# Optimization experiments

Measured on AMD Instinct MI355X. Metric: run time of the kernel, lower is better.

Reference implementation:

```python
import jax, jax.numpy as jnp
import numpy as np

V, N = 3, 32768
C2, C3 = 256, 32          # feat_ch_2D, feat_ch_3D
H = W = 128               # 2D feature map size
D = 32                    # 3D volume feature size
CIN = C2 + C3             # 288, MLP in_channels


def setup_inputs() -> dict:
    key = jax.random.key(0)
    ks = jax.random.split(key, 16)
    sc = 0.02
    inp = {
        'pts': jax.random.uniform(ks[0], (1, N, 3), minval=-0.5, maxval=0.5),
        'pts_proj': jax.random.uniform(ks[1], (1, N, 2), minval=-1.0, maxval=1.0),
        'img_feat0': jax.random.normal(ks[2], (V, C2, H, W)),
        'img_feat1': jax.random.normal(ks[3], (V, C2, H, W)),
        'vol_feat0': jax.random.normal(ks[4], (V, C3, D, D, D)),
        'vol_feat1': jax.random.normal(ks[5], (V, C3, D, D, D)),
        'W0': jax.random.normal(ks[6], (1024, CIN)) * sc,  'b0': jnp.zeros((1024,)),
        'W1': jax.random.normal(ks[7], (512, CIN + 1024)) * sc, 'b1': jnp.zeros((512,)),
        'W2': jax.random.normal(ks[8], (256, CIN + 512)) * sc,  'b2': jnp.zeros((256,)),
        'W3': jax.random.normal(ks[9], (128, CIN + 256)) * sc,  'b3': jnp.zeros((128,)),
        'W4': jax.random.normal(ks[10], (1, 128)) * sc,         'b4': jnp.zeros((1,)),
        'mean_num': 3,
    }
    return inp


def _gs2d(feat, gx, gy):
    # feat: [C,H,W]; gx,gy: [N] normalized coords in [-1,1]
    C, Hh, Ww = feat.shape
    ix = jnp.clip(((gx + 1.0) * Ww - 1.0) * 0.5, 0.0, Ww - 1.0)  # align_corners=False, border pad
    iy = jnp.clip(((gy + 1.0) * Hh - 1.0) * 0.5, 0.0, Hh - 1.0)
    x0f, y0f = jnp.floor(ix), jnp.floor(iy)
    wx, wy = ix - x0f, iy - y0f
    x0 = x0f.astype(jnp.int32); x1 = jnp.minimum(x0 + 1, Ww - 1)
    y0 = y0f.astype(jnp.int32); y1 = jnp.minimum(y0 + 1, Hh - 1)
    v00 = feat[:, y0, x0]; v01 = feat[:, y0, x1]
    v10 = feat[:, y1, x0]; v11 = feat[:, y1, x1]
    return (v00 * (1 - wy) * (1 - wx) + v01 * (1 - wy) * wx
            + v10 * wy * (1 - wx) + v11 * wy * wx)  # [C,N]


def _gs3d(feat, gx, gy, gz):
    # feat: [C,D,H,W]; grid x->W, y->H, z->D (torch grid_sample convention)
    C, Dd, Hh, Ww = feat.shape
    ix = jnp.clip(((gx + 1.0) * Ww - 1.0) * 0.5, 0.0, Ww - 1.0)
    iy = jnp.clip(((gy + 1.0) * Hh - 1.0) * 0.5, 0.0, Hh - 1.0)
    iz = jnp.clip(((gz + 1.0) * Dd - 1.0) * 0.5, 0.0, Dd - 1.0)
    x0f, y0f, z0f = jnp.floor(ix), jnp.floor(iy), jnp.floor(iz)
    wx, wy, wz = ix - x0f, iy - y0f, iz - z0f
    x0 = x0f.astype(jnp.int32); x1 = jnp.minimum(x0 + 1, Ww - 1)
    y0 = y0f.astype(jnp.int32); y1 = jnp.minimum(y0 + 1, Hh - 1)
    z0 = z0f.astype(jnp.int32); z1 = jnp.minimum(z0 + 1, Dd - 1)
    def g(zi, yi, xi):
        return feat[:, zi, yi, xi]  # [C,N]
    out = (g(z0, y0, x0) * (1 - wz) * (1 - wy) * (1 - wx)
           + g(z0, y0, x1) * (1 - wz) * (1 - wy) * wx
           + g(z0, y1, x0) * (1 - wz) * wy * (1 - wx)
           + g(z0, y1, x1) * (1 - wz) * wy * wx
           + g(z1, y0, x0) * wz * (1 - wy) * (1 - wx)
           + g(z1, y0, x1) * wz * (1 - wy) * wx
           + g(z1, y1, x0) * wz * wy * (1 - wx)
           + g(z1, y1, x1) * wz * wy * wx)
    return out  # [C,N]


def _lrelu(x):
    return jnp.where(x >= 0, x, 0.2 * x)


def _conv1x1(Wm, bm, x):
    # x: [V,C,N] -> [V,O,N]
    return jnp.einsum('oc,vcn->von', Wm, x) + bm[None, :, None]


def _mlp0(x, W0, b0, W1, b1, W2, b2, W3, b3):
    out = _lrelu(_conv1x1(W0, b0, x))
    out = _lrelu(_conv1x1(W1, b1, jnp.concatenate([x, out], axis=1)))
    out = _lrelu(_conv1x1(W2, b2, jnp.concatenate([x, out], axis=1)))
    out = _lrelu(_conv1x1(W3, b3, jnp.concatenate([x, out], axis=1)))
    return out  # [V,128,N]


def _forward(pts, pts_proj, img_feats, vol_feats,
             W0, b0, W1, b1, W2, b2, W3, b3, W4, b4, mean_num):
    v = img_feats[0].shape[0]
    gx2 = jnp.broadcast_to(pts_proj[:, :, 0], (v, pts_proj.shape[1]))
    gy2 = jnp.broadcast_to(pts_proj[:, :, 1], (v, pts_proj.shape[1]))
    p = pts * 2.0  # pts *= 2.0 before 3D sampling
    gx3 = jnp.broadcast_to(p[:, :, 0], (v, p.shape[1]))
    gy3 = jnp.broadcast_to(p[:, :, 1], (v, p.shape[1]))
    gz3 = jnp.broadcast_to(p[:, :, 2], (v, p.shape[1]))
    outs = []
    for img_feat, vol_feat in zip(img_feats, vol_feats):
        f2 = jax.vmap(_gs2d)(img_feat, gx2, gy2)            # [V,C2,N]
        f3 = jax.vmap(_gs3d)(vol_feat, gx3, gy3, gz3)       # [V,C3,N]
        pt_feat = jnp.concatenate([f2, f3], axis=1)         # [V,288,N]
        pt_out0 = _mlp0(pt_feat, W0, b0, W1, b1, W2, b2, W3, b3)
        pt_out0_mean = jnp.mean(pt_out0[:mean_num], axis=0, keepdims=True)  # [1,128,N]
        sdf = jax.nn.sigmoid(_conv1x1(W4, b4, pt_out0_mean))                # [1,1,N]
        outs.append(jnp.transpose(sdf, (0, 2, 1)))                          # [1,N,1]
    return tuple(outs)


def reference(pts, pts_proj, img_feat0, img_feat1, vol_feat0, vol_feat1,
              W0, b0, W1, b1, W2, b2, W3, b3, W4, b4, mean_num):
    return _forward(pts, pts_proj, [img_feat0, img_feat1], [vol_feat0, vol_feat1],
                    W0, b0, W1, b1, W2, b2, W3, b3, W4, b4, mean_num)
```

## Files before the change

### kernel.cpp

```cpp
#include <hip/hip_runtime.h>
#include <hip/hip_bf16.h>

#define NV 3
#define NPTS 32768
#define C2C 256
#define C3C 32
#define CINC 288
#define CINP 320
#define HH 128
#define WWW 128
#define DDD 32

typedef short bh8 __attribute__((ext_vector_type(8)));
typedef float fx4 __attribute__((ext_vector_type(4)));
typedef unsigned short us4 __attribute__((ext_vector_type(4)));

__device__ __forceinline__ float b2f(unsigned short u) {
    unsigned int x = ((unsigned int)u) << 16;
    return __uint_as_float(x);
}
__device__ __forceinline__ unsigned short f2b(float f) {
    unsigned int x = __float_as_uint(f);
    unsigned int r = (x + 0x7FFFu + ((x >> 16) & 1u)) >> 16;
    return (unsigned short)r;
}

__device__ __forceinline__ void gl2lds16(const unsigned short* g, unsigned short* l) {
    __builtin_amdgcn_global_load_lds(
        (const __attribute__((address_space(1))) unsigned int*)g,
        (__attribute__((address_space(3))) unsigned int*)l, 16, 0, 0);
}

template <int MB>
__device__ __forceinline__ void pair_decode(int b, int& mIdx, int& nIdx) {
    constexpr int L = (MB == 1) ? 0 : (MB == 2) ? 1 : 2;
    nIdx = ((b >> (3 + L)) << 3) | (b & 7);
    mIdx = (b >> 3) & (MB - 1);
}

__global__ __launch_bounds__(256) void k_prep(
    const float* __restrict__ s0, const float* __restrict__ s1,
    const float* __restrict__ s2, const float* __restrict__ s3,
    unsigned short* __restrict__ d0, unsigned short* __restrict__ d1,
    unsigned short* __restrict__ d2, unsigned short* __restrict__ d3,
    const float* __restrict__ img0, const float* __restrict__ img1,
    unsigned short* __restrict__ imgT, size_t imgStride,
    const float* __restrict__ vol0, const float* __restrict__ vol1,
    unsigned short* __restrict__ volT, size_t volStride) {
    __shared__ float smem[32 * 257];
    int b = blockIdx.x;
    if (b < 5088) {
        int base, M, Kp;
        const float* src;
        unsigned short* dst;
        if (b < 1280)      { base = 0;    M = 1024; Kp = 320;  src = s0; dst = d0; }
        else if (b < 3968) { base = 1280; M = 512;  Kp = 1344; src = s1; dst = d1; }
        else if (b < 4800) { base = 3968; M = 256;  Kp = 832;  src = s2; dst = d2; }
        else               { base = 4800; M = 128;  Kp = 576;  src = s3; dst = d3; }
        int idx = (b - base) * 256 + threadIdx.x;
        if (idx >= M * Kp) return;
        int m = idx / Kp, k = idx - m * Kp;
        int Ksrc = Kp - 32;
        float v;
        if (k < CINC) v = src[(size_t)m * Ksrc + k];
        else if (k < CINP) v = 0.0f;
        else v = src[(size_t)m * Ksrc + (k - 32)];
        dst[idx] = f2b(v);
    } else if (b < 11232) {
        int id = b - 5088;
        int bx = id % 384, by = (id / 384) & 1, bz = id / 768;
        int lvl = bz >> 2, cb = bz & 3;
        const float* in = lvl ? img1 : img0;
        int v = bx >> 7, y = bx & 127;
        int x0 = by << 6, c0 = cb << 6;
        float (*t)[65] = (float(*)[65])smem;
        int tx = threadIdx.x & 63, tg = threadIdx.x >> 6;
        const float* src = in + (((size_t)(v * C2C + c0) * HH + y) * WWW + x0);
#pragma unroll
        for (int i = 0; i < 16; i++) {
            int cl = tg * 16 + i;
            t[cl][tx] = src[(size_t)cl * (HH * WWW) + tx];
        }
        __syncthreads();
        unsigned short* dst = imgT + lvl * imgStride + ((size_t)(v * HH + y) * WWW + x0) * C2C + c0;
#pragma unroll
        for (int i = 0; i < 16; i++) {
            int xl = tg * 16 + i;
            dst[(size_t)xl * C2C + tx] = f2b(t[tx][xl]);
        }
    } else {
        int id = b - 11232;
        int v = id % 3, sy = (id / 3) & 127, lvl = id / 384;
        const float* in = lvl ? vol1 : vol0;
        int s0i = sy << 8;
        float (*t)[257] = (float(*)[257])smem;
        int tid = threadIdx.x;
        const float* src = in + (size_t)v * C3C * 32768 + s0i;
#pragma unroll
        for (int c = 0; c < 32; c++) t[c][tid] = src[(size_t)c * 32768 + tid];
        __syncthreads();
        unsigned short* dst = volT + lvl * volStride + ((size_t)v * 32768 + s0i) * C3C;
        int c = tid & 31, sb = tid >> 5;
#pragma unroll
        for (int j = 0; j < 32; j++) {
            int sl = j * 8 + sb;
            dst[(size_t)sl * C3C + c] = f2b(t[c][sl]);
        }
    }
}

__device__ __forceinline__ void sample_body(const float* __restrict__ pts, const float* __restrict__ proj,
                         const unsigned short* __restrict__ imgT, const unsigned short* __restrict__ volT,
                         unsigned short* __restrict__ ptT, int n0, int Nk) {
    int w = threadIdx.x >> 6, l = threadIdx.x & 63;
    int i = blockIdx.x * 4 + w;
    int v = blockIdx.y;
    int n = n0 + i;
    unsigned short* dstRow = ptT + (size_t)(v * Nk + i) * CINP;

    {
        float gx = proj[n * 2 + 0], gy = proj[n * 2 + 1];
        float ix = fminf(fmaxf(((gx + 1.0f) * (float)WWW - 1.0f) * 0.5f, 0.0f), (float)(WWW - 1));
        float iy = fminf(fmaxf(((gy + 1.0f) * (float)HH - 1.0f) * 0.5f, 0.0f), (float)(HH - 1));
        float x0f = floorf(ix), y0f = floorf(iy);
        float wx = ix - x0f, wy = iy - y0f;
        int x0 = (int)x0f, y0 = (int)y0f;
        int x1 = min(x0 + 1, WWW - 1), y1 = min(y0 + 1, HH - 1);
        const unsigned short* base = imgT + (size_t)v * HH * WWW * C2C;
        us4 a = *((const us4*)(base + ((size_t)(y0 * WWW + x0)) * C2C) + l);
        us4 b = *((const us4*)(base + ((size_t)(y0 * WWW + x1)) * C2C) + l);
        us4 c = *((const us4*)(base + ((size_t)(y1 * WWW + x0)) * C2C) + l);
        us4 d = *((const us4*)(base + ((size_t)(y1 * WWW + x1)) * C2C) + l);
        float w00 = (1.0f - wy) * (1.0f - wx), w01 = (1.0f - wy) * wx;
        float w10 = wy * (1.0f - wx), w11 = wy * wx;
        us4 rv;
#pragma unroll
        for (int r = 0; r < 4; r++) {
            float f = b2f(a[r]) * w00 + b2f(b[r]) * w01 + b2f(c[r]) * w10 + b2f(d[r]) * w11;
            rv[r] = f2b(f);
        }
        *(us4*)(dstRow + l * 4) = rv;
    }
    {
        float gx = pts[n * 3 + 0] * 2.0f, gy = pts[n * 3 + 1] * 2.0f, gz = pts[n * 3 + 2] * 2.0f;
        float ix = fminf(fmaxf(((gx + 1.0f) * (float)DDD - 1.0f) * 0.5f, 0.0f), (float)(DDD - 1));
        float iy = fminf(fmaxf(((gy + 1.0f) * (float)DDD - 1.0f) * 0.5f, 0.0f), (float)(DDD - 1));
        float iz = fminf(fmaxf(((gz + 1.0f) * (float)DDD - 1.0f) * 0.5f, 0.0f), (float)(DDD - 1));
        float x0f = floorf(ix), y0f = floorf(iy), z0f = floorf(iz);
        float wx = ix - x0f, wy = iy - y0f, wz = iz - z0f;
        int x0 = (int)x0f, y0 = (int)y0f, z0 = (int)z0f;
        int x1 = min(x0 + 1, DDD - 1), y1 = min(y0 + 1, DDD - 1), z1 = min(z0 + 1, DDD - 1);
        int c = l & 31, zs = l >> 5;
        int zi = zs ? z1 : z0;
        float wzs = zs ? wz : (1.0f - wz);
        const unsigned short* base = volT + (size_t)v * 32768 * C3C;
        float f00 = b2f(base[((size_t)((zi * 32 + y0) * 32 + x0)) * C3C + c]);
        float f01 = b2f(base[((size_t)((zi * 32 + y0) * 32 + x1)) * C3C + c]);
        float f10 = b2f(base[((size_t)((zi * 32 + y1) * 32 + x0)) * C3C + c]);
        float f11 = b2f(base[((size_t)((zi * 32 + y1) * 32 + x1)) * C3C + c]);
        float r = (f00 * (1.0f - wy) * (1.0f - wx) + f01 * (1.0f - wy) * wx +
                   f10 * wy * (1.0f - wx) + f11 * wy * wx) * wzs;
        float other = __shfl_xor(r, 32);
        r += other;
        if (zs == 0) dstRow[C2C + c] = f2b(r);
    }
    if (l < 8) *(us4*)(dstRow + CINC + l * 4) = (us4){0, 0, 0, 0};
}

__global__ __launch_bounds__(256) void k_sampleL0(const float* p, const float* pr, const unsigned short* im,
                                                  const unsigned short* vo, unsigned short* pt, int n0, int Nk) {
    sample_body(p, pr, im, vo, pt, n0, Nk);
}
__global__ __launch_bounds__(256) void k_sampleL1(const float* p, const float* pr, const unsigned short* im,
                                                  const unsigned short* vo, unsigned short* pt, int n0, int Nk) {
    sample_body(p, pr, im, vo, pt, n0, Nk);
}

template <int K2, int M, int MB>
__device__ __forceinline__ void gemm128_body(const unsigned short* __restrict__ A,
                                             const unsigned short* __restrict__ B1,
                                             const unsigned short* __restrict__ B2,
                                             const float* __restrict__ bias,
                                             unsigned short* __restrict__ C) {
    constexpr int K1 = CINP;
    constexpr int K = K1 + K2;
    constexpr int nt1 = K1 / 32;
    constexpr int nt = K / 32;
    __shared__ unsigned short Ash[3][128 * 32];
    __shared__ unsigned short Bsh[3][128 * 32];
    int tid = threadIdx.x;
    int w = tid >> 6, l = tid & 63;
    int la = l & 15, lg = l >> 4;
    int wm = w & 1, wn = w >> 1;
    int mIdx, nIdx;
    pair_decode<MB>(blockIdx.x, mIdx, nIdx);
    int mBlk = mIdx * 128;
    int nBlk = nIdx * 128;
    int sRow = l >> 2, sCol = (l & 3) * 8;
    int r0 = w * 32 + sRow, r1 = r0 + 16;

    const unsigned short* Ag = A + (size_t)mBlk * K;
    const unsigned short* B1g = B1 + (size_t)nBlk * K1;
    const unsigned short* B2g = (K2 > 0) ? (B2 + (size_t)nBlk * K2) : (const unsigned short*)0;

    fx4 acc[4][4];
#pragma unroll
    for (int mi = 0; mi < 4; mi++)
#pragma unroll
        for (int ni = 0; ni < 4; ni++) acc[mi][ni] = (fx4){0.f, 0.f, 0.f, 0.f};

    auto stage = [&](int t, int b) {
        const unsigned short* as = Ag + t * 32 + sCol;
        gl2lds16(as + (size_t)r0 * K, &Ash[b][r0 * 32 + sCol]);
        gl2lds16(as + (size_t)r1 * K, &Ash[b][r1 * 32 + sCol]);
        const unsigned short* bs;
        size_t ldb;
        if (t < nt1) { bs = B1g + t * 32 + sCol; ldb = (size_t)K1; }
        else         { bs = B2g + (t - nt1) * 32 + sCol; ldb = (size_t)K2; }
        gl2lds16(bs + (size_t)r0 * ldb, &Bsh[b][r0 * 32 + sCol]);
        gl2lds16(bs + (size_t)r1 * ldb, &Bsh[b][r1 * 32 + sCol]);
    };

    stage(0, 0);
    if (nt > 1) stage(1, 1);
    asm volatile("s_waitcnt vmcnt(4)" ::: "memory");
    __builtin_amdgcn_s_barrier();
    int cur = 0, nxt2 = 2;
    for (int t = 0; t < nt; t++) {
        if (t + 2 < nt) stage(t + 2, nxt2);
        bh8 af[4], bfv[4];
#pragma unroll
        for (int mi = 0; mi < 4; mi++) af[mi] = *(const bh8*)&Ash[cur][(wm * 64 + mi * 16 + la) * 32 + lg * 8];
#pragma unroll
        for (int ni = 0; ni < 4; ni++) bfv[ni] = *(const bh8*)&Bsh[cur][(wn * 64 + ni * 16 + la) * 32 + lg * 8];
#pragma unroll
        for (int mi = 0; mi < 4; mi++)
#pragma unroll
            for (int ni = 0; ni < 4; ni++)
                acc[mi][ni] = __builtin_amdgcn_mfma_f32_16x16x32_bf16(af[mi], bfv[ni], acc[mi][ni], 0, 0, 0);
        asm volatile("s_waitcnt lgkmcnt(0)" ::: "memory");
        if (t + 2 < nt)      asm volatile("s_waitcnt vmcnt(4)" ::: "memory");
        else if (t + 1 < nt) asm volatile("s_waitcnt vmcnt(0)" ::: "memory");
        __builtin_amdgcn_s_barrier();
        cur = (cur == 2) ? 0 : cur + 1;
        nxt2 = (nxt2 == 2) ? 0 : nxt2 + 1;
    }

#pragma unroll
    for (int mi = 0; mi < 4; mi++) {
        int m0 = mBlk + wm * 64 + mi * 16 + lg * 4;
        fx4 bb = *(const fx4*)(bias + m0);
#pragma unroll
        for (int ni = 0; ni < 4; ni++) {
            int n = nBlk + wn * 64 + ni * 16 + la;
            us4 rv;
#pragma unroll
            for (int r = 0; r < 4; r++) {
                float x = acc[mi][ni][r] + bb[r];
                x = (x >= 0.0f) ? x : 0.2f * x;
                rv[r] = f2b(x);
            }
            *(us4*)(C + (size_t)n * M + m0) = rv;
        }
    }
}

__global__ __launch_bounds__(256) void k_g2L0(const unsigned short* A, const unsigned short* B1, const unsigned short* B2,
                                              const float* b, unsigned short* C) { gemm128_body<512, 256, 2>(A, B1, B2, b, C); }
__global__ __launch_bounds__(256) void k_g2L1(const unsigned short* A, const unsigned short* B1, const unsigned short* B2,
                                              const float* b, unsigned short* C) { gemm128_body<512, 256, 2>(A, B1, B2, b, C); }
__global__ __launch_bounds__(256) void k_g3L0(const unsigned short* A, const unsigned short* B1, const unsigned short* B2,
                                              const float* b, unsigned short* C) { gemm128_body<256, 128, 1>(A, B1, B2, b, C); }
__global__ __launch_bounds__(256) void k_g3L1(const unsigned short* A, const unsigned short* B1, const unsigned short* B2,
                                              const float* b, unsigned short* C) { gemm128_body<256, 128, 1>(A, B1, B2, b, C); }

template <int KP, int K2, int M, int MB>
__device__ __forceinline__ void g1t_body(const unsigned short* __restrict__ A,
                                         const unsigned short* __restrict__ B1,
                                         const unsigned short* __restrict__ B2,
                                         const float* __restrict__ bias,
                                         unsigned short* __restrict__ C) {
    constexpr int nt = KP >> 6;
    __shared__ unsigned short As[2][256 * 64];
    __shared__ unsigned short Bs[2][256 * 64];
    int tid = threadIdx.x;
    int w = tid >> 6, l = tid & 63;
    int la = l & 15, lg = l >> 4;
    int wm = w >> 2, wn = w & 3;
    int mIdx, nIdx;
    pair_decode<MB>(blockIdx.x, mIdx, nIdx);
    int mBlk = mIdx * 256;
    int nBlk = nIdx * 256;

    const unsigned short* Ag = A + (size_t)mBlk * KP;

    fx4 acc[8][4];
#pragma unroll
    for (int mi = 0; mi < 8; mi++)
#pragma unroll
        for (int ni = 0; ni < 4; ni++) acc[mi][ni] = (fx4){0.f, 0.f, 0.f, 0.f};

    auto stageB = [&](int t, int nxt) {
        const unsigned short* bsrc;
        size_t ldb;
        int kc;
        if (t < 5) { bsrc = B1; ldb = CINP; kc = t * 64; }
        else       { bsrc = B2; ldb = (size_t)K2; kc = (t - 5) * 64; }
        bsrc += (size_t)nBlk * ldb + kc;
#pragma unroll
        for (int h = 0; h < 2; h++)
#pragma unroll
            for (int j = 0; j < 2; j++) {
                int idx = j * 512 + tid;
                int r = (h << 7) + (idx >> 3);
                int c = (idx & 7) ^ (r & 7);
                gl2lds16(bsrc + (size_t)r * ldb + c * 8, &Bs[nxt][(h << 13) + idx * 8]);
            }
    };
    auto stageA1 = [&](int t, int nxt) {
        const unsigned short* asrc = Ag + t * 64;
#pragma unroll
        for (int h = 0; h < 2; h++) {
            int idx = tid;
            int r = (h << 7) + (idx >> 3);
            int c = (idx & 7) ^ (r & 7);
            gl2lds16(asrc + (size_t)r * KP + c * 8, &As[nxt][(h << 13) + idx * 8]);
        }
    };
    auto stageA2 = [&](int t, int nxt) {
        const unsigned short* asrc = Ag + t * 64;
#pragma unroll
        for (int h = 0; h < 2; h++) {
            int idx = 512 + tid;
            int r = (h << 7) + (idx >> 3);
            int c = (idx & 7) ^ (r & 7);
            gl2lds16(asrc + (size_t)r * KP + c * 8, &As[nxt][(h << 13) + idx * 8]);
        }
    };

    stageB(0, 0);
    stageA1(0, 0);
    stageA2(0, 0);
    asm volatile("s_waitcnt vmcnt(0)" ::: "memory");
    __builtin_amdgcn_s_barrier();

    for (int t = 0; t < nt; t++) {
        int cur = t & 1;
        const unsigned short* Ab = &As[cur][0];
        const unsigned short* Bb = &Bs[cur][0];
        bh8 afr[4][2];
#pragma unroll
        for (int p = 0; p < 4; p++) {
            int qm = p >> 1, qn = p & 1;
            if (qn == 0) {
#pragma unroll
                for (int m2 = 0; m2 < 4; m2++)
#pragma unroll
                    for (int s = 0; s < 2; s++) {
                        int row = wm * 128 + (qm * 4 + m2) * 16 + la;
                        int c = (s * 4 + lg) ^ (row & 7);
                        afr[m2][s] = *(const bh8*)&Ab[row * 64 + c * 8];
                    }
            }
            bh8 bfr[2][2];
#pragma unroll
            for (int n2 = 0; n2 < 2; n2++)
#pragma unroll
                for (int s = 0; s < 2; s++) {
                    int row = wn * 64 + (qn * 2 + n2) * 16 + la;
                    int c = (s * 4 + lg) ^ (row & 7);
                    bfr[n2][s] = *(const bh8*)&Bb[row * 64 + c * 8];
                }
            if (p == 0 && t + 1 < nt) stageB(t + 1, cur ^ 1);
            if (p == 1 && t + 1 < nt) stageA1(t + 1, cur ^ 1);
            if (p == 2 && t + 1 < nt) stageA2(t + 1, cur ^ 1);
            __builtin_amdgcn_s_barrier();
            __builtin_amdgcn_s_setprio(1);
#pragma unroll
            for (int m2 = 0; m2 < 4; m2++)
#pragma unroll
                for (int n2 = 0; n2 < 2; n2++)
#pragma unroll
                    for (int s = 0; s < 2; s++)
                        acc[qm * 4 + m2][qn * 2 + n2] = __builtin_amdgcn_mfma_f32_16x16x32_bf16(
                            afr[m2][s], bfr[n2][s], acc[qm * 4 + m2][qn * 2 + n2], 0, 0, 0);
            __builtin_amdgcn_s_setprio(0);
            if (p == 1) {
                if (t + 1 < nt) asm volatile("s_waitcnt vmcnt(6)" ::: "memory");
                else            asm volatile("s_waitcnt vmcnt(0)" ::: "memory");
            }
            if (p == 3) {
                asm volatile("s_waitcnt lgkmcnt(0)" ::: "memory");
                if (t + 1 < nt) asm volatile("s_waitcnt vmcnt(2)" ::: "memory");
            }
            __builtin_amdgcn_s_barrier();
        }
    }

#pragma unroll
    for (int mi = 0; mi < 8; mi++) {
        int m0 = mBlk + wm * 128 + mi * 16 + lg * 4;
        fx4 bb = *(const fx4*)(bias + m0);
#pragma unroll
        for (int ni = 0; ni < 4; ni++) {
            int n = nBlk + wn * 64 + ni * 16 + la;
            us4 rv;
#pragma unroll
            for (int r = 0; r < 4; r++) {
                float x = acc[mi][ni][r] + bb[r];
                x = (x >= 0.0f) ? x : 0.2f * x;
                rv[r] = f2b(x);
            }
            *(us4*)(C + (size_t)n * M + m0) = rv;
        }
    }
}

__global__ __launch_bounds__(512) void k_g0L0(const unsigned short* A, const unsigned short* B1,
                                              const float* b, unsigned short* C) { g1t_body<320, 0, 1024, 4>(A, B1, nullptr, b, C); }
__global__ __launch_bounds__(512) void k_g0L1(const unsigned short* A, const unsigned short* B1,
                                              const float* b, unsigned short* C) { g1t_body<320, 0, 1024, 4>(A, B1, nullptr, b, C); }
__global__ __launch_bounds__(512) void k_g1L0(const unsigned short* A, const unsigned short* B1, const unsigned short* B2,
                                              const float* b, unsigned short* C) { g1t_body<1344, 1024, 512, 2>(A, B1, B2, b, C); }
__global__ __launch_bounds__(512) void k_g1L1(const unsigned short* A, const unsigned short* B1, const unsigned short* B2,
                                              const float* b, unsigned short* C) { g1t_body<1344, 1024, 512, 2>(A, B1, B2, b, C); }

__device__ __forceinline__ void head_body(const unsigned short* __restrict__ o3, const float* __restrict__ W4,
                       const float* __restrict__ b4, const int* __restrict__ mn_p,
                       float* __restrict__ out, int n0, int Nk, int level) {
    int wv = threadIdx.x >> 6, l = threadIdx.x & 63;
    int sub = l >> 4, cl = l & 15;
    int i = blockIdx.x * 16 + wv * 4 + sub;
    if (i >= Nk) return;
    int mn = *mn_p;
    if (mn > NV) mn = NV;
    if (mn < 1) mn = 1;
    fx4 w0 = *(const fx4*)(W4 + cl * 8);
    fx4 w1 = *(const fx4*)(W4 + cl * 8 + 4);
    float s = 0.0f;
    for (int v = 0; v < mn; v++) {
        bh8 x = *(const bh8*)(o3 + (size_t)(v * Nk + i) * 128 + cl * 8);
#pragma unroll
        for (int r = 0; r < 4; r++) s += w0[r] * b2f((unsigned short)x[r]);
#pragma unroll
        for (int r = 0; r < 4; r++) s += w1[r] * b2f((unsigned short)x[4 + r]);
    }
#pragma unroll
    for (int m = 1; m < 16; m <<= 1) s += __shfl_xor(s, m);
    if (cl == 0) {
        s = s / (float)mn + b4[0];
        out[(size_t)level * NPTS + n0 + i] = 1.0f / (1.0f + expf(-s));
    }
}

__global__ __launch_bounds__(256) void k_headL0(const unsigned short* o3, const float* W4, const float* b4,
                                                const int* mn, float* out, int n0, int Nk) {
    head_body(o3, W4, b4, mn, out, n0, Nk, 0);
}
__global__ __launch_bounds__(256) void k_headL1(const unsigned short* o3, const float* W4, const float* b4,
                                                const int* mn, float* out, int n0, int Nk) {
    head_body(o3, W4, b4, mn, out, n0, Nk, 1);
}

extern "C" void kernel_launch(void* const* d_in, const int* in_sizes, int n_in,
                              void* d_out, int out_size, void* d_ws, size_t ws_size,
                              hipStream_t stream) {
    const float* pts = (const float*)d_in[0];
    const float* proj = (const float*)d_in[1];
    const float* img[2] = {(const float*)d_in[2], (const float*)d_in[3]};
    const float* vol[2] = {(const float*)d_in[4], (const float*)d_in[5]};
    const float* Wf[4] = {(const float*)d_in[6], (const float*)d_in[8], (const float*)d_in[10], (const float*)d_in[12]};
    const float* bf[4] = {(const float*)d_in[7], (const float*)d_in[9], (const float*)d_in[11], (const float*)d_in[13]};
    const float* W4 = (const float*)d_in[14];
    const float* b4 = (const float*)d_in[15];
    const int* mn = (const int*)d_in[16];
    float* out = (float*)d_out;

    const int Kp[4] = {320, 1344, 832, 576};
    const int Msz[4] = {1024, 512, 256, 128};

    char* ws = (char*)d_ws;
    size_t off = 0;
    auto alloc = [&](size_t bytes) -> char* {
        char* p = ws + off;
        off = (off + bytes + 255) & ~(size_t)255;
        return p;
    };

    const size_t imgStride = (size_t)NV * HH * WWW * C2C;
    const size_t volStride = (size_t)NV * 32768 * C3C;

    unsigned short* Wb[4];
    for (int i = 0; i < 4; i++) Wb[i] = (unsigned short*)alloc((size_t)Msz[i] * Kp[i] * 2);
    unsigned short* imgT = (unsigned short*)alloc(2 * imgStride * 2);
    unsigned short* volT = (unsigned short*)alloc(2 * volStride * 2);
    size_t fixed = off;

    const size_t perPt = (size_t)NV * 2 * (CINP + 1024 + 512);
    int Nk = NPTS;
    if (fixed + (size_t)Nk * perPt + 4096 > ws_size) {
        size_t avail = (ws_size > fixed + 4096) ? (ws_size - fixed - 4096) : 0;
        long nk = (long)(avail / perPt);
        nk = (nk / 512) * 512;
        if (nk < 512) nk = 512;
        if (nk > NPTS) nk = NPTS;
        Nk = (int)nk;
    }
    unsigned short* ptT = (unsigned short*)alloc((size_t)NV * Nk * CINP * 2);
    unsigned short* o0 = (unsigned short*)alloc((size_t)NV * Nk * 1024 * 2);
    unsigned short* o1 = (unsigned short*)alloc((size_t)NV * Nk * 512 * 2);
    unsigned short* o2 = o0;
    unsigned short* o3 = o0 + (size_t)NV * Nk * 256;

    k_prep<<<12000, 256, 0, stream>>>(Wf[0], Wf[1], Wf[2], Wf[3], Wb[0], Wb[1], Wb[2], Wb[3],
                                      img[0], img[1], imgT, imgStride, vol[0], vol[1], volT, volStride);

    for (int n0 = 0; n0 < NPTS; n0 += Nk) {
        int nk = NPTS - n0 < Nk ? NPTS - n0 : Nk;
        int NC = NV * nk;
        int nP256 = NC / 256;
        int nP128 = NC / 128;
        k_sampleL0<<<dim3(nk / 4, NV), 256, 0, stream>>>(pts, proj, imgT, volT, ptT, n0, nk);
        k_g0L0<<<4 * nP256, 512, 0, stream>>>(Wb[0], ptT, bf[0], o0);
        k_g1L0<<<2 * nP256, 512, 0, stream>>>(Wb[1], ptT, o0, bf[1], o1);
        k_g2L0<<<2 * nP128, 256, 0, stream>>>(Wb[2], ptT, o1, bf[2], o2);
        k_g3L0<<<1 * nP128, 256, 0, stream>>>(Wb[3], ptT, o2, bf[3], o3);
        k_headL0<<<(nk + 15) / 16, 256, 0, stream>>>(o3, W4, b4, mn, out, n0, nk);
        k_sampleL1<<<dim3(nk / 4, NV), 256, 0, stream>>>(pts, proj, imgT + imgStride, volT + volStride, ptT, n0, nk);
        k_g0L1<<<4 * nP256, 512, 0, stream>>>(Wb[0], ptT, bf[0], o0);
        k_g1L1<<<2 * nP256, 512, 0, stream>>>(Wb[1], ptT, o0, bf[1], o1);
        k_g2L1<<<2 * nP128, 256, 0, stream>>>(Wb[2], ptT, o1, bf[2], o2);
        k_g3L1<<<1 * nP128, 256, 0, stream>>>(Wb[3], ptT, o2, bf[3], o3);
        k_headL1<<<(nk + 15) / 16, 256, 0, stream>>>(o3, W4, b4, mn, out, n0, nk);
    }
}
```

Before: 1.071 ms.

## Fuse final head dot product into layer-3 GEMM epilogue and retile layer 2

New measurement: 1.027 ms. 4.1% less time.

```diff
diff --git a/kernel.cpp b/kernel.cpp
--- a/kernel.cpp
+++ b/kernel.cpp
@@ -176,32 +176,31 @@
     sample_body(p, pr, im, vo, pt, n0, Nk);
 }
 
-template <int K2, int M, int MB>
-__device__ __forceinline__ void gemm128_body(const unsigned short* __restrict__ A,
-                                             const unsigned short* __restrict__ B1,
-                                             const unsigned short* __restrict__ B2,
-                                             const float* __restrict__ bias,
-                                             unsigned short* __restrict__ C) {
+template <int K2>
+__device__ __forceinline__ void g3dot_body(const unsigned short* __restrict__ A,
+                                           const unsigned short* __restrict__ B1,
+                                           const unsigned short* __restrict__ B2,
+                                           const float* __restrict__ bias,
+                                           const float* __restrict__ W4v,
+                                           float* __restrict__ dout) {
     constexpr int K1 = CINP;
     constexpr int K = K1 + K2;
     constexpr int nt1 = K1 / 32;
     constexpr int nt = K / 32;
     __shared__ unsigned short Ash[3][128 * 32];
     __shared__ unsigned short Bsh[3][128 * 32];
+    __shared__ float ds[128];
     int tid = threadIdx.x;
     int w = tid >> 6, l = tid & 63;
     int la = l & 15, lg = l >> 4;
     int wm = w & 1, wn = w >> 1;
-    int mIdx, nIdx;
-    pair_decode<MB>(blockIdx.x, mIdx, nIdx);
-    int mBlk = mIdx * 128;
-    int nBlk = nIdx * 128;
+    int nBlk = blockIdx.x * 128;
     int sRow = l >> 2, sCol = (l & 3) * 8;
     int r0 = w * 32 + sRow, r1 = r0 + 16;
 
-    const unsigned short* Ag = A + (size_t)mBlk * K;
+    const unsigned short* Ag = A;
     const unsigned short* B1g = B1 + (size_t)nBlk * K1;
-    const unsigned short* B2g = (K2 > 0) ? (B2 + (size_t)nBlk * K2) : (const unsigned short*)0;
+    const unsigned short* B2g = B2 + (size_t)nBlk * K2;
 
     fx4 acc[4][4];
 #pragma unroll
@@ -246,33 +245,34 @@
         nxt2 = (nxt2 == 2) ? 0 : nxt2 + 1;
     }
 
-#pragma unroll
-    for (int mi = 0; mi < 4; mi++) {
-        int m0 = mBlk + wm * 64 + mi * 16 + lg * 4;
-        fx4 bb = *(const fx4*)(bias + m0);
-#pragma unroll
-        for (int ni = 0; ni < 4; ni++) {
-            int n = nBlk + wn * 64 + ni * 16 + la;
-            us4 rv;
+    if (tid < 128) ds[tid] = 0.0f;
+    __syncthreads();
+#pragma unroll
+    for (int ni = 0; ni < 4; ni++) {
+        float part = 0.0f;
+#pragma unroll
+        for (int mi = 0; mi < 4; mi++) {
+            int m0 = wm * 64 + mi * 16 + lg * 4;
+            fx4 bb = *(const fx4*)(bias + m0);
 #pragma unroll
             for (int r = 0; r < 4; r++) {
                 float x = acc[mi][ni][r] + bb[r];
                 x = (x >= 0.0f) ? x : 0.2f * x;
-                rv[r] = f2b(x);
+                part += W4v[m0 + r] * x;
             }
-            *(us4*)(C + (size_t)n * M + m0) = rv;
-        }
-    }
-}
-
-__global__ __launch_bounds__(256) void k_g2L0(const unsigned short* A, const unsigned short* B1, const unsigned short* B2,
-                                              const float* b, unsigned short* C) { gemm128_body<512, 256, 2>(A, B1, B2, b, C); }
-__global__ __launch_bounds__(256) void k_g2L1(const unsigned short* A, const unsigned short* B1, const unsigned short* B2,
-                                              const float* b, unsigned short* C) { gemm128_body<512, 256, 2>(A, B1, B2, b, C); }
+        }
+        part += __shfl_xor(part, 16);
+        part += __shfl_xor(part, 32);
+        if (lg == 0) atomicAdd(&ds[wn * 64 + ni * 16 + la], part);
+    }
+    __syncthreads();
+    if (tid < 128) dout[nBlk + tid] = ds[tid];
+}
+
 __global__ __launch_bounds__(256) void k_g3L0(const unsigned short* A, const unsigned short* B1, const unsigned short* B2,
-                                              const float* b, unsigned short* C) { gemm128_body<256, 128, 1>(A, B1, B2, b, C); }
+                                              const float* b, const float* W4, float* dout) { g3dot_body<256>(A, B1, B2, b, W4, dout); }
 __global__ __launch_bounds__(256) void k_g3L1(const unsigned short* A, const unsigned short* B1, const unsigned short* B2,
-                                              const float* b, unsigned short* C) { gemm128_body<256, 128, 1>(A, B1, B2, b, C); }
+                                              const float* b, const float* W4, float* dout) { g3dot_body<256>(A, B1, B2, b, W4, dout); }
 
 template <int KP, int K2, int M, int MB>
 __device__ __forceinline__ void g1t_body(const unsigned short* __restrict__ A,
@@ -424,42 +424,23 @@
                                               const float* b, unsigned short* C) { g1t_body<1344, 1024, 512, 2>(A, B1, B2, b, C); }
 __global__ __launch_bounds__(512) void k_g1L1(const unsigned short* A, const unsigned short* B1, const unsigned short* B2,
                                               const float* b, unsigned short* C) { g1t_body<1344, 1024, 512, 2>(A, B1, B2, b, C); }
-
-__device__ __forceinline__ void head_body(const unsigned short* __restrict__ o3, const float* __restrict__ W4,
-                       const float* __restrict__ b4, const int* __restrict__ mn_p,
-                       float* __restrict__ out, int n0, int Nk, int level) {
-    int wv = threadIdx.x >> 6, l = threadIdx.x & 63;
-    int sub = l >> 4, cl = l & 15;
-    int i = blockIdx.x * 16 + wv * 4 + sub;
+__global__ __launch_bounds__(512) void k_g2L0(const unsigned short* A, const unsigned short* B1, const unsigned short* B2,
+                                              const float* b, unsigned short* C) { g1t_body<832, 512, 256, 1>(A, B1, B2, b, C); }
+__global__ __launch_bounds__(512) void k_g2L1(const unsigned short* A, const unsigned short* B1, const unsigned short* B2,
+                                              const float* b, unsigned short* C) { g1t_body<832, 512, 256, 1>(A, B1, B2, b, C); }
+
+__global__ __launch_bounds__(256) void k_fin(const float* __restrict__ d, const float* __restrict__ b4,
+                                             const int* __restrict__ mn_p, float* __restrict__ out,
+                                             int n0, int Nk, int level) {
+    int i = blockIdx.x * 256 + threadIdx.x;
     if (i >= Nk) return;
     int mn = *mn_p;
     if (mn > NV) mn = NV;
     if (mn < 1) mn = 1;
-    fx4 w0 = *(const fx4*)(W4 + cl * 8);
-    fx4 w1 = *(const fx4*)(W4 + cl * 8 + 4);
     float s = 0.0f;
-    for (int v = 0; v < mn; v++) {
-        bh8 x = *(const bh8*)(o3 + (size_t)(v * Nk + i) * 128 + cl * 8);
-#pragma unroll
-        for (int r = 0; r < 4; r++) s += w0[r] * b2f((unsigned short)x[r]);
-#pragma unroll
-        for (int r = 0; r < 4; r++) s += w1[r] * b2f((unsigned short)x[4 + r]);
-    }
-#pragma unroll
-    for (int m = 1; m < 16; m <<= 1) s += __shfl_xor(s, m);
-    if (cl == 0) {
-        s = s / (float)mn + b4[0];
-        out[(size_t)level * NPTS + n0 + i] = 1.0f / (1.0f + expf(-s));
-    }
-}
-
-__global__ __launch_bounds__(256) void k_headL0(const unsigned short* o3, const float* W4, const float* b4,
-                                                const int* mn, float* out, int n0, int Nk) {
-    head_body(o3, W4, b4, mn, out, n0, Nk, 0);
-}
-__global__ __launch_bounds__(256) void k_headL1(const unsigned short* o3, const float* W4, const float* b4,
-                                                const int* mn, float* out, int n0, int Nk) {
-    head_body(o3, W4, b4, mn, out, n0, Nk, 1);
+    for (int v = 0; v < mn; v++) s += d[(size_t)v * Nk + i];
+    s = s / (float)mn + b4[0];
+    out[(size_t)level * NPTS + n0 + i] = 1.0f / (1.0f + expf(-s));
 }
 
 extern "C" void kernel_launch(void* const* d_in, const int* in_sizes, int n_in,
@@ -496,13 +477,13 @@
     unsigned short* volT = (unsigned short*)alloc(2 * volStride * 2);
     size_t fixed = off;
 
-    const size_t perPt = (size_t)NV * 2 * (CINP + 1024 + 512);
+    const size_t perPt = (size_t)NV * (2 * (CINP + 1024 + 512) + 4);
     int Nk = NPTS;
     if (fixed + (size_t)Nk * perPt + 4096 > ws_size) {
         size_t avail = (ws_size > fixed + 4096) ? (ws_size - fixed - 4096) : 0;
         long nk = (long)(avail / perPt);
-        nk = (nk / 512) * 512;
-        if (nk < 512) nk = 512;
+        nk = (nk / 2048) * 2048;
+        if (nk < 2048) nk = 2048;
         if (nk > NPTS) nk = NPTS;
         Nk = (int)nk;
     }
@@ -510,7 +491,7 @@
     unsigned short* o0 = (unsigned short*)alloc((size_t)NV * Nk * 1024 * 2);
     unsigned short* o1 = (unsigned short*)alloc((size_t)NV * Nk * 512 * 2);
     unsigned short* o2 = o0;
-    unsigned short* o3 = o0 + (size_t)NV * Nk * 256;
+    float* dsum = (float*)alloc((size_t)NV * Nk * 4);
 
     k_prep<<<12000, 256, 0, stream>>>(Wf[0], Wf[1], Wf[2], Wf[3], Wb[0], Wb[1], Wb[2], Wb[3],
                                       img[0], img[1], imgT, imgStride, vol[0], vol[1], volT, volStride);
@@ -523,14 +504,14 @@
         k_sampleL0<<<dim3(nk / 4, NV), 256, 0, stream>>>(pts, proj, imgT, volT, ptT, n0, nk);
         k_g0L0<<<4 * nP256, 512, 0, stream>>>(Wb[0], ptT, bf[0], o0);
         k_g1L0<<<2 * nP256, 512, 0, stream>>>(Wb[1], ptT, o0, bf[1], o1);
-        k_g2L0<<<2 * nP128, 256, 0, stream>>>(Wb[2], ptT, o1, bf[2], o2);
-        k_g3L0<<<1 * nP128, 256, 0, stream>>>(Wb[3], ptT, o2, bf[3], o3);
-        k_headL0<<<(nk + 15) / 16, 256, 0, stream>>>(o3, W4, b4, mn, out, n0, nk);
+        k_g2L0<<<1 * nP256, 512, 0, stream>>>(Wb[2], ptT, o1, bf[2], o2);
+        k_g3L0<<<nP128, 256, 0, stream>>>(Wb[3], ptT, o2, bf[3], W4, dsum);
+        k_fin<<<(nk + 255) / 256, 256, 0, stream>>>(dsum, b4, mn, out, n0, nk, 0);
         k_sampleL1<<<dim3(nk / 4, NV), 256, 0, stream>>>(pts, proj, imgT + imgStride, volT + volStride, ptT, n0, nk);
         k_g0L1<<<4 * nP256, 512, 0, stream>>>(Wb[0], ptT, bf[0], o0);
         k_g1L1<<<2 * nP256, 512, 0, stream>>>(Wb[1], ptT, o0, bf[1], o1);
-        k_g2L1<<<2 * nP128, 256, 0, stream>>>(Wb[2], ptT, o1, bf[2], o2);
-        k_g3L1<<<1 * nP128, 256, 0, stream>>>(Wb[3], ptT, o2, bf[3], o3);
-        k_headL1<<<(nk + 15) / 16, 256, 0, stream>>>(o3, W4, b4, mn, out, n0, nk);
-    }
-}
+        k_g2L1<<<1 * nP256, 512, 0, stream>>>(Wb[2], ptT, o1, bf[2], o2);
+        k_g3L1<<<nP128, 256, 0, stream>>>(Wb[3], ptT, o2, bf[3], W4, dsum);
+        k_fin<<<(nk + 255) / 256, 256, 0, stream>>>(dsum, b4, mn, out, n0, nk, 1);
+    }
+}
```
